# Optimization experiments

Measured on AMD Instinct MI355X. Metric: run time of the kernel, lower is better.

Reference implementation:

```python
import jax, jax.numpy as jnp
import numpy as np

D, H, DH, L, DFF, V, K = 512, 8, 64, 6, 2048, 256, 5
N = 10240
TAU = 0.1
EPS = 1e-5


def _ln(x, w, b):
    m = x.mean(-1, keepdims=True)
    v = ((x - m) ** 2).mean(-1, keepdims=True)
    return (x - m) * jax.lax.rsqrt(v + EPS) * w + b


def _attn(q_in, kv_in, inw, inb, ow, ob):
    # q_in: [Q, D], kv_in: [M, D]; standard PyTorch MultiheadAttention math
    wq, wk, wv = jnp.split(inw, 3, 0)
    bq, bk, bv = jnp.split(inb, 3)
    q = (q_in @ wq.T + bq).reshape(-1, H, DH)
    k = (kv_in @ wk.T + bk).reshape(-1, H, DH)
    v = (kv_in @ wv.T + bv).reshape(-1, H, DH)
    s = jnp.einsum('qhd,mhd->hqm', q, k) / np.float32(np.sqrt(DH))
    o = jnp.einsum('hqm,mhd->qhd', jax.nn.softmax(s, -1), v).reshape(-1, D)
    return o @ ow.T + ob


def setup_inputs() -> dict:
    key = jax.random.key(0)
    ks = iter(jax.random.split(key, 64))

    def w(shape):
        return jax.random.normal(next(ks), shape, jnp.float32) * 0.02

    inp = {
        'input_bytes': jax.random.randint(next(ks), (N,), 0, V, jnp.int32),
        'emb': w((V, D)),
        'alpha': jnp.float32(0.5),
        'enc_inw': w((L, 3 * D, D)), 'enc_inb': w((L, 3 * D)),
        'enc_ow': w((L, D, D)), 'enc_ob': w((L, D)),
        'enc_w1': w((L, DFF, D)), 'enc_b1': w((L, DFF)),
        'enc_w2': w((L, D, DFF)), 'enc_b2': w((L, D)),
        'enc_ln1w': jnp.ones((L, D)), 'enc_ln1b': jnp.zeros((L, D)),
        'enc_ln2w': jnp.ones((L, D)), 'enc_ln2b': jnp.zeros((L, D)),
        'dec_sa_inw': w((L, 3 * D, D)), 'dec_sa_inb': w((L, 3 * D)),
        'dec_sa_ow': w((L, D, D)), 'dec_sa_ob': w((L, D)),
        'dec_ca_inw': w((L, 3 * D, D)), 'dec_ca_inb': w((L, 3 * D)),
        'dec_ca_ow': w((L, D, D)), 'dec_ca_ob': w((L, D)),
        'dec_w1': w((L, DFF, D)), 'dec_b1': w((L, DFF)),
        'dec_w2': w((L, D, DFF)), 'dec_b2': w((L, D)),
        'dec_ln1w': jnp.ones((L, D)), 'dec_ln1b': jnp.zeros((L, D)),
        'dec_ln2w': jnp.ones((L, D)), 'dec_ln2b': jnp.zeros((L, D)),
        'dec_ln3w': jnp.ones((L, D)), 'dec_ln3b': jnp.zeros((L, D)),
        'out_w': w((V, D)), 'out_b': w((V,)),
    }
    return inp


def reference(input_bytes, emb, alpha, enc_inw, enc_inb, enc_ow, enc_ob,
              enc_w1, enc_b1, enc_w2, enc_b2, enc_ln1w, enc_ln1b, enc_ln2w, enc_ln2b,
              dec_sa_inw, dec_sa_inb, dec_sa_ow, dec_sa_ob,
              dec_ca_inw, dec_ca_inb, dec_ca_ow, dec_ca_ob,
              dec_w1, dec_b1, dec_w2, dec_b2,
              dec_ln1w, dec_ln1b, dec_ln2w, dec_ln2b, dec_ln3w, dec_ln3b,
              out_w, out_b):
    P = input_bytes.shape[0] // K
    patches = input_bytes[:P * K].reshape(P, K)            # fixed k-byte patching
    x = emb[patches].mean(1)                               # mean-pooled patch embeddings [P, D]
    # ---- TransformerEncoder (post-LN, relu FFN, no dropout at eval) ----
    for l in range(L):
        x = _ln(x + _attn(x, x, enc_inw[l], enc_inb[l], enc_ow[l], enc_ob[l]), enc_ln1w[l], enc_ln1b[l])
        ff = jax.nn.relu(x @ enc_w1[l].T + enc_b1[l]) @ enc_w2[l].T + enc_b2[l]
        x = _ln(x + ff, enc_ln2w[l], enc_ln2b[l])
    encoded = x                                            # [P, D]
    # ---- gating + embedding mix (vectorized over the per-patch loop) ----
    gate = jnp.linalg.norm(encoded, axis=-1) > TAU
    tok = emb[patches[:, -1]]
    x = jnp.where(gate[:, None], alpha * encoded + (1.0 - alpha) * tok, tok)  # [P, D]
    # ---- TransformerDecoder: each patch is an independent length-1 target;
    #      self-attn over a single token reduces to out_proj(V(x));
    #      cross-attn attends to the full encoded memory (as in the original loop) ----
    for l in range(L):
        wv = dec_sa_inw[l][2 * D:]
        bv = dec_sa_inb[l][2 * D:]
        sa = (x @ wv.T + bv) @ dec_sa_ow[l].T + dec_sa_ob[l]
        x = _ln(x + sa, dec_ln1w[l], dec_ln1b[l])
        ca = _attn(x, encoded, dec_ca_inw[l], dec_ca_inb[l], dec_ca_ow[l], dec_ca_ob[l])
        x = _ln(x + ca, dec_ln2w[l], dec_ln2b[l])
        ff = jax.nn.relu(x @ dec_w1[l].T + dec_b1[l]) @ dec_w2[l].T + dec_b2[l]
        x = _ln(x + ff, dec_ln3w[l], dec_ln3b[l])
    return x @ out_w.T + out_b                             # [P, V]
```

## Files before the change

### kernel.cpp

```cpp
#include <hip/hip_runtime.h>
#include <hip/hip_bf16.h>
#include <math.h>

#define DD   512
#define HN   8
#define DHD  64
#define LL   6
#define DFF_ 2048
#define VV   256
#define KB_  5
#define PP   2048
#define EPS_ 1e-5f
#define TAU_ 0.1f
#define NS   4
#define KVS  (PP / NS)

typedef __attribute__((ext_vector_type(8))) short bf16x8;
typedef __attribute__((ext_vector_type(4))) short bf16x4;
typedef __attribute__((ext_vector_type(4))) float f32x4;

__device__ __forceinline__ float wave_sum(float v) {
#pragma unroll
  for (int m = 32; m >= 1; m >>= 1) v += __shfl_xor(v, m, 64);
  return v;
}

__device__ __forceinline__ unsigned short f2bf(float f) {
  unsigned u = __float_as_uint(f);
  u += 0x7FFF + ((u >> 16) & 1);
  return (unsigned short)(u >> 16);
}

__device__ __forceinline__ bf16x8 cvt8(float4 a, float4 b) {
  bf16x8 v;
  v[0] = (short)f2bf(a.x); v[1] = (short)f2bf(a.y);
  v[2] = (short)f2bf(a.z); v[3] = (short)f2bf(a.w);
  v[4] = (short)f2bf(b.x); v[5] = (short)f2bf(b.y);
  v[6] = (short)f2bf(b.z); v[7] = (short)f2bf(b.w);
  return v;
}

__device__ __forceinline__ void gload16(const void* g, void* l) {
  __builtin_amdgcn_global_load_lds(
      (const __attribute__((address_space(1))) unsigned int*)g,
      (__attribute__((address_space(3))) unsigned int*)l, 16, 0, 0);
}

#define NSEG 55
struct CvtSeg { const float* src; short* dst; int n; };
struct CvtArgs { CvtSeg seg[NSEG]; };

__global__ __launch_bounds__(256) void convert_bf16_kernel(CvtArgs a) {
  const CvtSeg sg = a.seg[blockIdx.y];
  const int i = ((int)blockIdx.x * 256 + (int)threadIdx.x) * 8;
  if (i >= sg.n) return;
  const float4 x0 = *(const float4*)(sg.src + i);
  const float4 x1 = *(const float4*)(sg.src + i + 4);
  *(bf16x8*)(sg.dst + i) = cvt8(x0, x1);
}

__global__ __launch_bounds__(256) void transpose_wv_kernel(const float* __restrict__ sa_inw,
                                                           short* __restrict__ wvt) {
  __shared__ float t[64][65];
  const int l = blockIdx.z;
  const float* S = sa_inw + (size_t)l * 3 * DD * DD + (size_t)2 * DD * DD;
  short* D = wvt + (size_t)l * DD * DD;
  const int bo = blockIdx.y * 64;
  const int bi = blockIdx.x * 64;
  const int r = (int)threadIdx.x >> 2;
  const int c0 = ((int)threadIdx.x & 3) * 16;
#pragma unroll
  for (int j = 0; j < 16; j += 4)
    *(float4*)&t[r][c0 + j] = *(const float4*)&S[(size_t)(bo + r) * DD + bi + c0 + j];
  __syncthreads();
  bf16x8 o0, o1;
#pragma unroll
  for (int j = 0; j < 8; ++j) o0[j] = (short)f2bf(t[c0 + j][r]);
#pragma unroll
  for (int j = 0; j < 8; ++j) o1[j] = (short)f2bf(t[c0 + 8 + j][r]);
  short* dp = &D[(size_t)(bi + r) * DD + bo + c0];
  *(bf16x8*)dp = o0;
  *(bf16x8*)(dp + 8) = o1;
}

__global__ __launch_bounds__(256) void sa_bias_kernel(const float* __restrict__ sa_inb,
                                                      const float* __restrict__ sa_ow,
                                                      const float* __restrict__ sa_ob,
                                                      float* __restrict__ bc) {
  const int gid = (int)blockIdx.x * 4 + ((int)threadIdx.x >> 6);
  const int l = gid >> 9, n = gid & 511;
  const int lane = (int)threadIdx.x & 63;
  const float* wo = sa_ow + (size_t)l * DD * DD + (size_t)n * DD + lane * 8;
  const float* bv = sa_inb + (size_t)l * 3 * DD + 2 * DD + lane * 8;
  float s = 0.f;
#pragma unroll
  for (int j = 0; j < 8; ++j) s += wo[j] * bv[j];
  s = wave_sum(s);
  if (lane == 0) bc[(size_t)l * DD + n] = s + sa_ob[(size_t)l * DD + n];
}

__global__ __launch_bounds__(256) void gemm_wc_kernel(const short* __restrict__ WoBase,
                                                      size_t astr,
                                                      const short* __restrict__ WvT,
                                                      short* __restrict__ Wc) {
  constexpr int BK = 64;
  __shared__ short As[64 * BK];
  __shared__ short Bs[64 * BK];
  const int l = blockIdx.z;
  const short* A = WoBase + (size_t)l * astr;
  const short* W = WvT + (size_t)l * DD * DD;
  short* C = Wc + (size_t)l * DD * DD;
  const int tid = (int)threadIdx.x;
  const int lane = tid & 63;
  const int wid = tid >> 6;
  const int wm = (wid >> 1) * 32;
  const int wn = (wid & 1) * 32;
  const int bm = blockIdx.y * 64;
  const int bn = blockIdx.x * 64;
  const int fr = lane & 15;
  const int kq = lane >> 4;
  const int rs = fr & 7;
  const int srow = lane >> 3;
  const int scg = (lane & 7) ^ srow;

  f32x4 acc[2][2];
#pragma unroll
  for (int i = 0; i < 2; ++i)
#pragma unroll
    for (int j = 0; j < 2; ++j) acc[i][j] = (f32x4){0.f, 0.f, 0.f, 0.f};

  for (int k0 = 0; k0 < DD; k0 += BK) {
    __syncthreads();
#pragma unroll
    for (int is = 0; is < 2; ++is) {
      const int ib = is * 4 + wid;
      gload16(&A[(size_t)(bm + ib * 8 + srow) * DD + k0 + scg * 8], &As[ib * 512]);
      gload16(&W[(size_t)(bn + ib * 8 + srow) * DD + k0 + scg * 8], &Bs[ib * 512]);
    }
    __syncthreads();
#pragma unroll
    for (int s = 0; s < 2; ++s) {
      const int cg = s * 4 + kq;
      const int co = (cg ^ rs) * 8;
      bf16x8 af[2], bf[2];
#pragma unroll
      for (int i = 0; i < 2; ++i) af[i] = *(const bf16x8*)&As[(wm + i * 16 + fr) * BK + co];
#pragma unroll
      for (int j = 0; j < 2; ++j) bf[j] = *(const bf16x8*)&Bs[(wn + j * 16 + fr) * BK + co];
#pragma unroll
      for (int i = 0; i < 2; ++i)
#pragma unroll
        for (int j = 0; j < 2; ++j)
          acc[i][j] = __builtin_amdgcn_mfma_f32_16x16x32_bf16(af[i], bf[j], acc[i][j], 0, 0, 0);
    }
  }
  const int cr = (lane >> 4) * 4;
#pragma unroll
  for (int j = 0; j < 2; ++j) {
    const int col = bn + wn + j * 16 + fr;
#pragma unroll
    for (int i = 0; i < 2; ++i)
#pragma unroll
      for (int r = 0; r < 4; ++r)
        C[(size_t)(bm + wm + i * 16 + cr + r) * DD + col] = (short)f2bf(acc[i][j][r]);
  }
}

__global__ __launch_bounds__(256) void embed_mean_kernel(const int* __restrict__ bytes,
                                                         const float* __restrict__ emb,
                                                         float* __restrict__ x,
                                                         short* __restrict__ xb,
                                                         float* __restrict__ tok) {
  const int p = blockIdx.x;
  const int d = threadIdx.x * 2;
  float a0 = 0.f, a1 = 0.f;
  int last = 0;
#pragma unroll
  for (int k = 0; k < KB_; ++k) {
    const int idx = bytes[p * KB_ + k];
    last = idx;
    const float* e = emb + (size_t)idx * DD + d;
    a0 += e[0]; a1 += e[1];
  }
  a0 *= 0.2f; a1 *= 0.2f;
  x[(size_t)p * DD + d]     = a0;
  x[(size_t)p * DD + d + 1] = a1;
  xb[(size_t)p * DD + d]     = (short)f2bf(a0);
  xb[(size_t)p * DD + d + 1] = (short)f2bf(a1);
  const float* e = emb + (size_t)last * DD + d;
  tok[(size_t)p * DD + d]     = e[0];
  tok[(size_t)p * DD + d + 1] = e[1];
}

template <int BM, int BN, int NSPLIT, int RELU, int WF32, int WBF16, int QS>
__global__ __launch_bounds__(256) void gemm_gl_kernel(
    const short* __restrict__ A, int lda,
    const short* __restrict__ W, int ldw,
    const float* __restrict__ bias,
    float* __restrict__ Cf, short* __restrict__ Cb, int ldc, int Kd,
    size_t pstride) {
  constexpr int BK = 64;
  __shared__ short As[BM * BK];
  __shared__ short Bs[BN * BK];
  constexpr int WM = BM / 2, WN = BN / 2;
  constexpr int MF = WM / 16, NF = WN / 16;
  const int tid = (int)threadIdx.x;
  const int lane = tid & 63;
  const int wid = tid >> 6;
  const int wm = (wid >> 1) * WM;
  const int wn = (wid & 1) * WN;
  const int bm = blockIdx.y * BM;
  const int bn = blockIdx.x * BN;
  const int fr = lane & 15;
  const int kq = lane >> 4;
  const int rs = fr & 7;
  const int srow = lane >> 3;
  const int scg = (lane & 7) ^ srow;

  const int kz = (NSPLIT > 1) ? (int)blockIdx.z : 0;
  const int kbeg = kz * (Kd / NSPLIT);
  const int kend = kbeg + Kd / NSPLIT;

  f32x4 acc[MF][NF];
#pragma unroll
  for (int i = 0; i < MF; ++i)
#pragma unroll
    for (int j = 0; j < NF; ++j) acc[i][j] = (f32x4){0.f, 0.f, 0.f, 0.f};

  for (int k0 = kbeg; k0 < kend; k0 += BK) {
    __syncthreads();
#pragma unroll
    for (int is = 0; is < BM / 32; ++is) {
      const int ib = is * 4 + wid;
      gload16(&A[(size_t)(bm + ib * 8 + srow) * lda + k0 + scg * 8], &As[ib * 512]);
    }
#pragma unroll
    for (int is = 0; is < BN / 32; ++is) {
      const int ib = is * 4 + wid;
      gload16(&W[(size_t)(bn + ib * 8 + srow) * ldw + k0 + scg * 8], &Bs[ib * 512]);
    }
    __syncthreads();
#pragma unroll
    for (int s = 0; s < 2; ++s) {
      const int cg = s * 4 + kq;
      const int co = (cg ^ rs) * 8;
      bf16x8 af[MF], bf[NF];
#pragma unroll
      for (int i = 0; i < MF; ++i)
        af[i] = *(const bf16x8*)&As[(wm + i * 16 + fr) * BK + co];
#pragma unroll
      for (int j = 0; j < NF; ++j)
        bf[j] = *(const bf16x8*)&Bs[(wn + j * 16 + fr) * BK + co];
#pragma unroll
      for (int i = 0; i < MF; ++i)
#pragma unroll
        for (int j = 0; j < NF; ++j)
          acc[i][j] = __builtin_amdgcn_mfma_f32_16x16x32_bf16(af[i], bf[j], acc[i][j], 0, 0, 0);
    }
  }

  const int cr = (lane >> 4) * 4;
  if constexpr (NSPLIT > 1) {
    float* dst = Cf + (size_t)kz * pstride;
#pragma unroll
    for (int j = 0; j < NF; ++j) {
      const int col = bn + wn + j * 16 + fr;
#pragma unroll
      for (int i = 0; i < MF; ++i)
#pragma unroll
        for (int r = 0; r < 4; ++r)
          dst[(size_t)(bm + wm + i * 16 + cr + r) * ldc + col] = acc[i][j][r];
    }
  } else {
#pragma unroll
    for (int j = 0; j < NF; ++j) {
      const int col = bn + wn + j * 16 + fr;
      const float bb = bias[col];
      const float sc = (QS && col < DD) ? 0.125f : 1.f;
#pragma unroll
      for (int i = 0; i < MF; ++i) {
#pragma unroll
        for (int r = 0; r < 4; ++r) {
          float v = (acc[i][j][r] + bb) * sc;
          if (RELU) v = fmaxf(v, 0.f);
          const size_t idx = (size_t)(bm + wm + i * 16 + cr + r) * ldc + col;
          if (WF32) Cf[idx] = v;
          if (WBF16) Cb[idx] = (short)f2bf(v);
        }
      }
    }
  }
}

__global__ __launch_bounds__(256) void gemm_ca_kernel(
    const short* __restrict__ Aq, const short* __restrict__ Akv,
    const short* __restrict__ Wfull, const float* __restrict__ bias,
    short* __restrict__ Cb) {
  constexpr int BK = 64;
  __shared__ short As[64 * BK];
  __shared__ short Bs[64 * BK];
  const int bx = (int)blockIdx.x;
  const int part_kv = bx >= 8;
  const short* A = part_kv ? Akv : Aq;
  const int wrow0 = part_kv ? DD + (bx - 8) * 64 : bx * 64;
  const float sc = part_kv ? 1.f : 0.125f;
  const int tid = (int)threadIdx.x;
  const int lane = tid & 63;
  const int wid = tid >> 6;
  const int wm = (wid >> 1) * 32;
  const int wn = (wid & 1) * 32;
  const int bm = blockIdx.y * 64;
  const int fr = lane & 15;
  const int kq = lane >> 4;
  const int rs = fr & 7;
  const int srow = lane >> 3;
  const int scg = (lane & 7) ^ srow;

  f32x4 acc[2][2];
#pragma unroll
  for (int i = 0; i < 2; ++i)
#pragma unroll
    for (int j = 0; j < 2; ++j) acc[i][j] = (f32x4){0.f, 0.f, 0.f, 0.f};

  for (int k0 = 0; k0 < DD; k0 += BK) {
    __syncthreads();
#pragma unroll
    for (int is = 0; is < 2; ++is) {
      const int ib = is * 4 + wid;
      gload16(&A[(size_t)(bm + ib * 8 + srow) * DD + k0 + scg * 8], &As[ib * 512]);
      gload16(&Wfull[(size_t)(wrow0 + ib * 8 + srow) * DD + k0 + scg * 8], &Bs[ib * 512]);
    }
    __syncthreads();
#pragma unroll
    for (int s = 0; s < 2; ++s) {
      const int cg = s * 4 + kq;
      const int co = (cg ^ rs) * 8;
      bf16x8 af[2], bf[2];
#pragma unroll
      for (int i = 0; i < 2; ++i) af[i] = *(const bf16x8*)&As[(wm + i * 16 + fr) * BK + co];
#pragma unroll
      for (int j = 0; j < 2; ++j) bf[j] = *(const bf16x8*)&Bs[(wn + j * 16 + fr) * BK + co];
#pragma unroll
      for (int i = 0; i < 2; ++i)
#pragma unroll
        for (int j = 0; j < 2; ++j)
          acc[i][j] = __builtin_amdgcn_mfma_f32_16x16x32_bf16(af[i], bf[j], acc[i][j], 0, 0, 0);
    }
  }
  const int cr = (lane >> 4) * 4;
#pragma unroll
  for (int j = 0; j < 2; ++j) {
    const int col = wrow0 + wn + j * 16 + fr;
    const float bb = bias[col];
#pragma unroll
    for (int i = 0; i < 2; ++i)
#pragma unroll
      for (int r = 0; r < 4; ++r)
        Cb[(size_t)(bm + wm + i * 16 + cr + r) * (3 * DD) + col] =
            (short)f2bf((acc[i][j][r] + bb) * sc);
  }
}

__global__ __launch_bounds__(256) void flash_attn_mfma_kernel(const short* __restrict__ qkvb,
                                                              float* __restrict__ Opart,
                                                              float* __restrict__ stats) {
  constexpr int LS = 72;
  __shared__ short Ks[64 * LS];
  __shared__ short Vt[64 * LS];
  __shared__ short Ps[64 * LS];
  const int h = blockIdx.y;
  const int q0 = blockIdx.x * 64;
  const int sp = blockIdx.z;
  const int tid = (int)threadIdx.x;
  const int lane = tid & 63;
  const int wid = tid >> 6;
  const int fr = lane & 15;
  const int g = lane >> 4;
  const int kg = g * 8;

  bf16x8 qf[2];
  {
    const short* src = qkvb + (size_t)(q0 + wid * 16 + fr) * (3 * DD) + h * DHD + kg;
    qf[0] = *(const bf16x8*)src;
    qf[1] = *(const bf16x8*)(src + 32);
  }

  f32x4 acc_o[4];
#pragma unroll
  for (int df = 0; df < 4; ++df) acc_o[df] = (f32x4){0.f, 0.f, 0.f, 0.f};
  float mreg = -INFINITY, lsum = 0.f;

  const int sr8 = tid >> 3;
  const int sc8 = (tid & 7) * 8;
  const int vk2 = (tid & 31) * 2;
  const int vd8 = (tid >> 5) * 8;

  for (int t = 0; t < KVS / 64; ++t) {
    const int k0 = sp * KVS + t * 64;
    __syncthreads();
    {
#pragma unroll
      for (int p = 0; p < 64; p += 32)
        *(bf16x8*)&Ks[(sr8 + p) * LS + sc8] =
            *(const bf16x8*)&qkvb[(size_t)(k0 + sr8 + p) * (3 * DD) + DD + h * DHD + sc8];
      const short* vbase = qkvb + (size_t)(k0 + vk2) * (3 * DD) + 2 * DD + h * DHD + vd8;
      const bf16x8 v0 = *(const bf16x8*)vbase;
      const bf16x8 v1 = *(const bf16x8*)(vbase + 3 * DD);
#pragma unroll
      for (int j = 0; j < 8; ++j) {
        const unsigned pk = ((unsigned)(unsigned short)v0[j]) |
                            (((unsigned)(unsigned short)v1[j]) << 16);
        *(unsigned*)&Vt[(vd8 + j) * LS + vk2] = pk;
      }
    }
    __syncthreads();

    f32x4 st[4];
#pragma unroll
    for (int nf = 0; nf < 4; ++nf) st[nf] = (f32x4){0.f, 0.f, 0.f, 0.f};
    __builtin_amdgcn_s_setprio(1);
#pragma unroll
    for (int nf = 0; nf < 4; ++nf) {
      const bf16x8 kf0 = *(const bf16x8*)&Ks[(nf * 16 + fr) * LS + kg];
      const bf16x8 kf1 = *(const bf16x8*)&Ks[(nf * 16 + fr) * LS + kg + 32];
      st[nf] = __builtin_amdgcn_mfma_f32_16x16x32_bf16(kf0, qf[0], st[nf], 0, 0, 0);
      st[nf] = __builtin_amdgcn_mfma_f32_16x16x32_bf16(kf1, qf[1], st[nf], 0, 0, 0);
    }
    __builtin_amdgcn_s_setprio(0);

    float mx = st[0][0];
#pragma unroll
    for (int nf = 0; nf < 4; ++nf)
#pragma unroll
      for (int i = 0; i < 4; ++i) mx = fmaxf(mx, st[nf][i]);
    mx = fmaxf(mx, __shfl_xor(mx, 16, 64));
    mx = fmaxf(mx, __shfl_xor(mx, 32, 64));
    const float mn = fmaxf(mreg, mx);
    const float corr = __expf(mreg - mn);
    mreg = mn;
    float pv[4][4];
    float sum = 0.f;
#pragma unroll
    for (int nf = 0; nf < 4; ++nf)
#pragma unroll
      for (int i = 0; i < 4; ++i) {
        pv[nf][i] = __expf(st[nf][i] - mn);
        sum += pv[nf][i];
      }
    sum += __shfl_xor(sum, 16, 64);
    sum += __shfl_xor(sum, 32, 64);
    lsum = lsum * corr + sum;

    float corr_acc[4];
#pragma unroll
    for (int i = 0; i < 4; ++i)
      corr_acc[i] = __shfl(corr, (lane & 48) | (g * 4 + i), 64);
#pragma unroll
    for (int df = 0; df < 4; ++df) {
      acc_o[df][0] *= corr_acc[0]; acc_o[df][1] *= corr_acc[1];
      acc_o[df][2] *= corr_acc[2]; acc_o[df][3] *= corr_acc[3];
    }

#pragma unroll
    for (int nf = 0; nf < 4; ++nf) {
      bf16x4 pw;
#pragma unroll
      for (int i = 0; i < 4; ++i) pw[i] = (short)f2bf(pv[nf][i]);
      *(bf16x4*)&Ps[(wid * 16 + fr) * LS + nf * 16 + g * 4] = pw;
    }
    asm volatile("s_waitcnt lgkmcnt(0)" ::: "memory");

    const bf16x8 pa0 = *(const bf16x8*)&Ps[(wid * 16 + fr) * LS + kg];
    const bf16x8 pa1 = *(const bf16x8*)&Ps[(wid * 16 + fr) * LS + kg + 32];
    __builtin_amdgcn_s_setprio(1);
#pragma unroll
    for (int df = 0; df < 4; ++df) {
      const bf16x8 vb0 = *(const bf16x8*)&Vt[(df * 16 + fr) * LS + kg];
      const bf16x8 vb1 = *(const bf16x8*)&Vt[(df * 16 + fr) * LS + kg + 32];
      acc_o[df] = __builtin_amdgcn_mfma_f32_16x16x32_bf16(pa0, vb0, acc_o[df], 0, 0, 0);
      acc_o[df] = __builtin_amdgcn_mfma_f32_16x16x32_bf16(pa1, vb1, acc_o[df], 0, 0, 0);
    }
    __builtin_amdgcn_s_setprio(0);
  }

  const int orow = q0 + wid * 16 + g * 4;
#pragma unroll
  for (int df = 0; df < 4; ++df)
#pragma unroll
    for (int i = 0; i < 4; ++i)
      Opart[((size_t)sp * PP + orow + i) * DD + h * DHD + df * 16 + fr] = acc_o[df][i];
  if (g == 0) {
    const size_t si = (((size_t)sp * PP + q0 + wid * 16 + fr) * HN + h) * 2;
    stats[si]     = mreg;
    stats[si + 1] = lsum;
  }
}

__global__ __launch_bounds__(256) void attn_combine_kernel(const float* __restrict__ Opart,
                                                           const float* __restrict__ stats,
                                                           short* __restrict__ outb) {
  const int row = blockIdx.x;
  const int d = (int)threadIdx.x * 2;
  const int h = d >> 6;
  float m[NS], l[NS];
  float M = -INFINITY;
#pragma unroll
  for (int s = 0; s < NS; ++s) {
    const size_t si = (((size_t)s * PP + row) * HN + h) * 2;
    m[s] = stats[si]; l[s] = stats[si + 1];
    M = fmaxf(M, m[s]);
  }
  float L = 0.f, o0 = 0.f, o1 = 0.f;
#pragma unroll
  for (int s = 0; s < NS; ++s) {
    const float e = __expf(m[s] - M);
    L += l[s] * e;
    const float* op = Opart + ((size_t)s * PP + row) * DD + d;
    o0 += op[0] * e;
    o1 += op[1] * e;
  }
  const float inv = 1.f / L;
  outb[(size_t)row * DD + d]     = (short)f2bf(o0 * inv);
  outb[(size_t)row * DD + d + 1] = (short)f2bf(o1 * inv);
}

__global__ __launch_bounds__(256) void ln_residual_kernel(const float* __restrict__ xin,
                                                          const float* __restrict__ pA,
                                                          const float* __restrict__ pB,
                                                          const float* __restrict__ gb,
                                                          const float* __restrict__ w,
                                                          const float* __restrict__ b,
                                                          float* __restrict__ out,
                                                          short* __restrict__ outb) {
  const int row = blockIdx.x * 4 + (threadIdx.x >> 6);
  const int lane = threadIdx.x & 63;
  const size_t base = (size_t)row * DD + lane * 8;
  float v[8];
  {
    const float4 a0 = *(const float4*)&xin[base];
    const float4 a1 = *(const float4*)&xin[base + 4];
    const float4 r0 = *(const float4*)&pA[base];
    const float4 r1 = *(const float4*)&pA[base + 4];
    const float4 s0 = *(const float4*)&pB[base];
    const float4 s1 = *(const float4*)&pB[base + 4];
    const float4 g0 = *(const float4*)&gb[lane * 8];
    const float4 g1 = *(const float4*)&gb[lane * 8 + 4];
    v[0] = a0.x + r0.x + s0.x + g0.x; v[1] = a0.y + r0.y + s0.y + g0.y;
    v[2] = a0.z + r0.z + s0.z + g0.z; v[3] = a0.w + r0.w + s0.w + g0.w;
    v[4] = a1.x + r1.x + s1.x + g1.x; v[5] = a1.y + r1.y + s1.y + g1.y;
    v[6] = a1.z + r1.z + s1.z + g1.z; v[7] = a1.w + r1.w + s1.w + g1.w;
  }
  float sum = 0.f;
#pragma unroll
  for (int j = 0; j < 8; ++j) sum += v[j];
  sum = wave_sum(sum);
  const float mean = sum * (1.f / DD);
  float sq = 0.f;
#pragma unroll
  for (int j = 0; j < 8; ++j) { const float dd = v[j] - mean; sq += dd * dd; }
  sq = wave_sum(sq);
  const float rstd = rsqrtf(sq * (1.f / DD) + EPS_);
  const float* wp = w + lane * 8;
  const float* bp = b + lane * 8;
  float o[8];
#pragma unroll
  for (int j = 0; j < 8; ++j) o[j] = (v[j] - mean) * rstd * wp[j] + bp[j];
  *(float4*)&out[base] = *(float4*)&o[0];
  *(float4*)&out[base + 4] = *(float4*)&o[4];
  bf16x8 ob;
#pragma unroll
  for (int j = 0; j < 8; ++j) ob[j] = (short)f2bf(o[j]);
  *(bf16x8*)&outb[base] = ob;
}

__global__ __launch_bounds__(256) void gate_mix_kernel(const float* __restrict__ tok,
                                                       const float* __restrict__ alpha_p,
                                                       float* __restrict__ x,
                                                       short* __restrict__ xb,
                                                       short* __restrict__ encb) {
  const int row = blockIdx.x * 4 + (threadIdx.x >> 6);
  const int lane = threadIdx.x & 63;
  const size_t base = (size_t)row * DD + lane * 8;
  float e[8], t[8];
  {
    const float4 a0 = *(const float4*)&x[base];
    const float4 a1 = *(const float4*)&x[base + 4];
    const float4 b0 = *(const float4*)&tok[base];
    const float4 b1 = *(const float4*)&tok[base + 4];
    e[0] = a0.x; e[1] = a0.y; e[2] = a0.z; e[3] = a0.w;
    e[4] = a1.x; e[5] = a1.y; e[6] = a1.z; e[7] = a1.w;
    t[0] = b0.x; t[1] = b0.y; t[2] = b0.z; t[3] = b0.w;
    t[4] = b1.x; t[5] = b1.y; t[6] = b1.z; t[7] = b1.w;
  }
  bf16x8 eb;
#pragma unroll
  for (int j = 0; j < 8; ++j) eb[j] = (short)f2bf(e[j]);
  *(bf16x8*)&encb[base] = eb;
  float sq = 0.f;
#pragma unroll
  for (int j = 0; j < 8; ++j) sq += e[j] * e[j];
  sq = wave_sum(sq);
  const bool gate = sq > TAU_ * TAU_;
  const float a = *alpha_p;
  float o[8];
#pragma unroll
  for (int j = 0; j < 8; ++j) o[j] = gate ? (a * e[j] + (1.f - a) * t[j]) : t[j];
  *(float4*)&x[base] = *(float4*)&o[0];
  *(float4*)&x[base + 4] = *(float4*)&o[4];
  bf16x8 ob;
#pragma unroll
  for (int j = 0; j < 8; ++j) ob[j] = (short)f2bf(o[j]);
  *(bf16x8*)&xb[base] = ob;
}

__global__ __launch_bounds__(256) void out_combine_kernel(const float* __restrict__ P0,
                                                          const float* __restrict__ P1,
                                                          const float* __restrict__ bias,
                                                          float* __restrict__ out) {
  const size_t i = ((size_t)blockIdx.x * 256 + threadIdx.x) * 4;
  const int col = (int)(i % VV);
  const float4 a = *(const float4*)&P0[i];
  const float4 b = *(const float4*)&P1[i];
  const float4 c = *(const float4*)&bias[col];
  float4 o;
  o.x = a.x + b.x + c.x; o.y = a.y + b.y + c.y;
  o.z = a.z + b.z + c.z; o.w = a.w + b.w + c.w;
  *(float4*)&out[i] = o;
}

extern "C" void kernel_launch(void* const* d_in, const int* in_sizes, int n_in,
                              void* d_out, int out_size, void* d_ws, size_t ws_size,
                              hipStream_t stream) {
  const int*   bytes    = (const int*)d_in[0];
  const float* emb      = (const float*)d_in[1];
  const float* alpha    = (const float*)d_in[2];
  const float* enc_inw  = (const float*)d_in[3];
  const float* enc_inb  = (const float*)d_in[4];
  const float* enc_ow   = (const float*)d_in[5];
  const float* enc_ob   = (const float*)d_in[6];
  const float* enc_w1   = (const float*)d_in[7];
  const float* enc_b1   = (const float*)d_in[8];
  const float* enc_w2   = (const float*)d_in[9];
  const float* enc_b2   = (const float*)d_in[10];
  const float* enc_ln1w = (const float*)d_in[11];
  const float* enc_ln1b = (const float*)d_in[12];
  const float* enc_ln2w = (const float*)d_in[13];
  const float* enc_ln2b = (const float*)d_in[14];
  const float* dec_sa_inw = (const float*)d_in[15];
  const float* dec_sa_inb = (const float*)d_in[16];
  const float* dec_sa_ow  = (const float*)d_in[17];
  const float* dec_sa_ob  = (const float*)d_in[18];
  const float* dec_ca_inw = (const float*)d_in[19];
  const float* dec_ca_inb = (const float*)d_in[20];
  const float* dec_ca_ow  = (const float*)d_in[21];
  const float* dec_ca_ob  = (const float*)d_in[22];
  const float* dec_w1   = (const float*)d_in[23];
  const float* dec_b1   = (const float*)d_in[24];
  const float* dec_w2   = (const float*)d_in[25];
  const float* dec_b2   = (const float*)d_in[26];
  const float* dec_ln1w = (const float*)d_in[27];
  const float* dec_ln1b = (const float*)d_in[28];
  const float* dec_ln2w = (const float*)d_in[29];
  const float* dec_ln2b = (const float*)d_in[30];
  const float* dec_ln3w = (const float*)d_in[31];
  const float* dec_ln3b = (const float*)d_in[32];
  const float* out_w    = (const float*)d_in[33];
  const float* out_b    = (const float*)d_in[34];

  float* fp = (float*)d_ws;
  float* x     = fp;  fp += (size_t)PP * DD;
  float* tok   = fp;  fp += (size_t)PP * DD;
  float* Opart = fp;  fp += (size_t)NS * PP * DD;
  float* stats = fp;  fp += (size_t)NS * PP * HN * 2;
  float* tmpP  = fp;  fp += (size_t)2 * PP * DD;
  float* outP  = fp;  fp += (size_t)2 * PP * VV;
  float* bcbuf = fp;  fp += (size_t)LL * DD;
  short* sp = (short*)fp;
  short* x_bf    = sp;  sp += (size_t)PP * DD;
  short* enc_bf  = sp;  sp += (size_t)PP * DD;
  short* qkv_bf  = sp;  sp += (size_t)PP * 3 * DD;
  short* attno_bf= sp;  sp += (size_t)PP * DFF_;
  short* ffh_bf  = sp;  sp += (size_t)PP * DFF_;
  short* wvT     = sp;  sp += (size_t)LL * DD * DD;
  short* wcM     = sp;  sp += (size_t)LL * DD * DD;
  short* warena  = sp;

  CvtArgs ca;
  size_t eoff[LL][4], doff[LL][5], ooff;
  size_t dec_start = 0, dec_stride = 0;
  {
    int si = 0;
    size_t off = 0;
    const size_t n0 = 3 * DD * DD, n1 = DD * DD, n2 = (size_t)DFF_ * DD, n3 = (size_t)DD * DFF_;
    for (int l = 0; l < LL; ++l) {
      ca.seg[si++] = {enc_inw + (size_t)l * n0, warena + off, (int)n0}; eoff[l][0] = off; off += n0;
      ca.seg[si++] = {enc_ow  + (size_t)l * n1, warena + off, (int)n1}; eoff[l][1] = off; off += n1;
      ca.seg[si++] = {enc_w1  + (size_t)l * n2, warena + off, (int)n2}; eoff[l][2] = off; off += n2;
      ca.seg[si++] = {enc_w2  + (size_t)l * n3, warena + off, (int)n3}; eoff[l][3] = off; off += n3;
    }
    dec_start = off;
    for (int l = 0; l < LL; ++l) {
      const size_t o0 = off;
      ca.seg[si++] = {dec_sa_ow  + (size_t)l * n1, warena + off, (int)n1}; doff[l][0] = off; off += n1;
      ca.seg[si++] = {dec_ca_inw + (size_t)l * n0, warena + off, (int)n0}; doff[l][1] = off; off += n0;
      ca.seg[si++] = {dec_ca_ow  + (size_t)l * n1, warena + off, (int)n1}; doff[l][2] = off; off += n1;
      ca.seg[si++] = {dec_w1     + (size_t)l * n2, warena + off, (int)n2}; doff[l][3] = off; off += n2;
      ca.seg[si++] = {dec_w2     + (size_t)l * n3, warena + off, (int)n3}; doff[l][4] = off; off += n3;
      if (l == 0) dec_stride = off - o0; (void)o0;
    }
    ca.seg[si++] = {out_w, warena + off, VV * DD}; ooff = off;
  }

  const dim3 b256(256);
  const dim3 gFA(PP / 64, HN, NS);
  const dim3 gQKV(3 * DD / 64, PP / 128);
  const dim3 gFF1(DFF_ / 64, PP / 128);
  const dim3 gS(DD / 64, PP / 64, 2);
  const dim3 gCA(24, PP / 64);
  const dim3 gOUTg(VV / 64, PP / 64, 2);
  const size_t psD = (size_t)PP * DD;
  const size_t psV = (size_t)PP * VV;

  convert_bf16_kernel<<<dim3(512, NSEG), b256, 0, stream>>>(ca);
  transpose_wv_kernel<<<dim3(8, 8, LL), b256, 0, stream>>>(dec_sa_inw, wvT);
  sa_bias_kernel<<<(LL * DD) / 4, b256, 0, stream>>>(dec_sa_inb, dec_sa_ow, dec_sa_ob, bcbuf);
  gemm_wc_kernel<<<dim3(8, 8, LL), b256, 0, stream>>>(warena + dec_start, dec_stride, wvT, wcM);
  embed_mean_kernel<<<PP, b256, 0, stream>>>(bytes, emb, x, x_bf, tok);

  for (int l = 0; l < LL; ++l) {
    const float* inb = enc_inb + (size_t)l * 3 * DD;
    const float* ob  = enc_ob  + (size_t)l * DD;
    const float* b1  = enc_b1  + (size_t)l * DFF_;
    const float* b2  = enc_b2  + (size_t)l * DD;

    gemm_gl_kernel<128, 64, 1, 0, 0, 1, 1><<<gQKV, b256, 0, stream>>>(
        x_bf, DD, warena + eoff[l][0], DD, inb, nullptr, qkv_bf, 3 * DD, DD, 0);
    flash_attn_mfma_kernel<<<gFA, b256, 0, stream>>>(qkv_bf, Opart, stats);
    attn_combine_kernel<<<PP, b256, 0, stream>>>(Opart, stats, attno_bf);
    gemm_gl_kernel<64, 64, 2, 0, 1, 0, 0><<<gS, b256, 0, stream>>>(
        attno_bf, DD, warena + eoff[l][1], DD, nullptr, tmpP, nullptr, DD, DD, psD);
    ln_residual_kernel<<<PP / 4, b256, 0, stream>>>(
        x, tmpP, tmpP + psD, ob, enc_ln1w + (size_t)l * DD, enc_ln1b + (size_t)l * DD, x, x_bf);
    gemm_gl_kernel<128, 64, 1, 1, 0, 1, 0><<<gFF1, b256, 0, stream>>>(
        x_bf, DD, warena + eoff[l][2], DD, b1, nullptr, ffh_bf, DFF_, DD, 0);
    gemm_gl_kernel<64, 64, 2, 0, 1, 0, 0><<<gS, b256, 0, stream>>>(
        ffh_bf, DFF_, warena + eoff[l][3], DFF_, nullptr, tmpP, nullptr, DD, DFF_, psD);
    ln_residual_kernel<<<PP / 4, b256, 0, stream>>>(
        x, tmpP, tmpP + psD, b2, enc_ln2w + (size_t)l * DD, enc_ln2b + (size_t)l * DD, x, x_bf);
  }

  gate_mix_kernel<<<PP / 4, b256, 0, stream>>>(tok, alpha, x, x_bf, enc_bf);

  for (int l = 0; l < LL; ++l) {
    const float* ca_inb = dec_ca_inb + (size_t)l * 3 * DD;
    const float* ca_ob  = dec_ca_ob + (size_t)l * DD;
    const float* b1 = dec_b1 + (size_t)l * DFF_;
    const float* b2 = dec_b2 + (size_t)l * DD;

    gemm_gl_kernel<64, 64, 2, 0, 1, 0, 0><<<gS, b256, 0, stream>>>(
        x_bf, DD, wcM + (size_t)l * DD * DD, DD, nullptr, tmpP, nullptr, DD, DD, psD);
    ln_residual_kernel<<<PP / 4, b256, 0, stream>>>(
        x, tmpP, tmpP + psD, bcbuf + (size_t)l * DD,
        dec_ln1w + (size_t)l * DD, dec_ln1b + (size_t)l * DD, x, x_bf);

    gemm_ca_kernel<<<gCA, b256, 0, stream>>>(
        x_bf, enc_bf, warena + doff[l][1], ca_inb, qkv_bf);
    flash_attn_mfma_kernel<<<gFA, b256, 0, stream>>>(qkv_bf, Opart, stats);
    attn_combine_kernel<<<PP, b256, 0, stream>>>(Opart, stats, attno_bf);
    gemm_gl_kernel<64, 64, 2, 0, 1, 0, 0><<<gS, b256, 0, stream>>>(
        attno_bf, DD, warena + doff[l][2], DD, nullptr, tmpP, nullptr, DD, DD, psD);
    ln_residual_kernel<<<PP / 4, b256, 0, stream>>>(
        x, tmpP, tmpP + psD, ca_ob, dec_ln2w + (size_t)l * DD, dec_ln2b + (size_t)l * DD, x, x_bf);

    gemm_gl_kernel<128, 64, 1, 1, 0, 1, 0><<<gFF1, b256, 0, stream>>>(
        x_bf, DD, warena + doff[l][3], DD, b1, nullptr, ffh_bf, DFF_, DD, 0);
    gemm_gl_kernel<64, 64, 2, 0, 1, 0, 0><<<gS, b256, 0, stream>>>(
        ffh_bf, DFF_, warena + doff[l][4], DFF_, nullptr, tmpP, nullptr, DD, DFF_, psD);
    ln_residual_kernel<<<PP / 4, b256, 0, stream>>>(
        x, tmpP, tmpP + psD, b2, dec_ln3w + (size_t)l * DD, dec_ln3b + (size_t)l * DD, x, x_bf);
  }

  gemm_gl_kernel<64, 64, 2, 0, 1, 0, 0><<<gOUTg, b256, 0, stream>>>(
      x_bf, DD, warena + ooff, DD, nullptr, outP, nullptr, VV, DD, psV);
  out_combine_kernel<<<(PP * VV / 4) / 256, b256, 0, stream>>>(
      outP, outP + psV, out_b, (float*)d_out);
}
```

Measured before the change: 1.110 ms.

## Fuse split-KV attention combine into out-projection GEMM A-tile load

```diff
diff --git a/kernel.cpp b/kernel.cpp
--- a/kernel.cpp
+++ b/kernel.cpp
@@ -52,11 +52,14 @@
 
 __global__ __launch_bounds__(256) void convert_bf16_kernel(CvtArgs a) {
   const CvtSeg sg = a.seg[blockIdx.y];
-  const int i = ((int)blockIdx.x * 256 + (int)threadIdx.x) * 8;
+  const int i = ((int)blockIdx.x * 256 + (int)threadIdx.x) * 16;
   if (i >= sg.n) return;
   const float4 x0 = *(const float4*)(sg.src + i);
   const float4 x1 = *(const float4*)(sg.src + i + 4);
-  *(bf16x8*)(sg.dst + i) = cvt8(x0, x1);
+  const float4 x2 = *(const float4*)(sg.src + i + 8);
+  const float4 x3 = *(const float4*)(sg.src + i + 12);
+  *(bf16x8*)(sg.dst + i)     = cvt8(x0, x1);
+  *(bf16x8*)(sg.dst + i + 8) = cvt8(x2, x3);
 }
 
 __global__ __launch_bounds__(256) void transpose_wv_kernel(const float* __restrict__ sa_inw,
@@ -292,6 +295,114 @@
   }
 }
 
+__global__ __launch_bounds__(256) void gemm_ao_kernel(
+    const float* __restrict__ Opart, const float* __restrict__ stats,
+    const short* __restrict__ W, float* __restrict__ Cf, size_t pstride) {
+  constexpr int BK = 64;
+  __shared__ short As[64 * BK];
+  __shared__ short Bs[64 * BK];
+  const int tid = (int)threadIdx.x;
+  const int lane = tid & 63;
+  const int wid = tid >> 6;
+  const int wm = (wid >> 1) * 32;
+  const int wn = (wid & 1) * 32;
+  const int bm = blockIdx.y * 64;
+  const int bn = blockIdx.x * 64;
+  const int fr = lane & 15;
+  const int kq = lane >> 4;
+  const int rs = fr & 7;
+  const int srow = lane >> 3;
+  const int scg = (lane & 7) ^ srow;
+  const int arow = tid >> 2;
+  const int acg0 = (tid & 3) * 2;
+  const int ad0 = acg0 * 8;
+
+  const int kz = (int)blockIdx.z;
+  const int kbeg = kz * (DD / 2);
+
+  f32x4 acc[2][2];
+#pragma unroll
+  for (int i = 0; i < 2; ++i)
+#pragma unroll
+    for (int j = 0; j < 2; ++j) acc[i][j] = (f32x4){0.f, 0.f, 0.f, 0.f};
+
+  for (int t = 0; t < 4; ++t) {
+    const int k0 = kbeg + t * BK;
+    const int h = k0 >> 6;
+    __syncthreads();
+#pragma unroll
+    for (int is = 0; is < 2; ++is) {
+      const int ib = is * 4 + wid;
+      gload16(&W[(size_t)(bn + ib * 8 + srow) * DD + k0 + scg * 8], &Bs[ib * 512]);
+    }
+    {
+      const int row = bm + arow;
+      float mm[NS], ll[NS];
+      float M = -INFINITY;
+#pragma unroll
+      for (int s = 0; s < NS; ++s) {
+        const size_t si = (((size_t)s * PP + row) * HN + h) * 2;
+        mm[s] = stats[si]; ll[s] = stats[si + 1];
+        M = fmaxf(M, mm[s]);
+      }
+      float L = 0.f, e[NS];
+#pragma unroll
+      for (int s = 0; s < NS; ++s) { e[s] = __expf(mm[s] - M); L += ll[s] * e[s]; }
+      const float inv = 1.f / L;
+      float o[16];
+#pragma unroll
+      for (int j = 0; j < 16; ++j) o[j] = 0.f;
+#pragma unroll
+      for (int s = 0; s < NS; ++s) {
+        const float sc = e[s] * inv;
+        const float* op = Opart + ((size_t)s * PP + row) * DD + k0 + ad0;
+        const float4 a0 = *(const float4*)op;
+        const float4 a1 = *(const float4*)(op + 4);
+        const float4 a2 = *(const float4*)(op + 8);
+        const float4 a3 = *(const float4*)(op + 12);
+        o[0]  += a0.x * sc; o[1]  += a0.y * sc; o[2]  += a0.z * sc; o[3]  += a0.w * sc;
+        o[4]  += a1.x * sc; o[5]  += a1.y * sc; o[6]  += a1.z * sc; o[7]  += a1.w * sc;
+        o[8]  += a2.x * sc; o[9]  += a2.y * sc; o[10] += a2.z * sc; o[11] += a2.w * sc;
+        o[12] += a3.x * sc; o[13] += a3.y * sc; o[14] += a3.z * sc; o[15] += a3.w * sc;
+      }
+      bf16x8 lo, hi;
+#pragma unroll
+      for (int j = 0; j < 8; ++j) { lo[j] = (short)f2bf(o[j]); hi[j] = (short)f2bf(o[8 + j]); }
+      const int r7 = arow & 7;
+      *(bf16x8*)&As[arow * BK + ((acg0 ^ r7) << 3)]       = lo;
+      *(bf16x8*)&As[arow * BK + (((acg0 + 1) ^ r7) << 3)] = hi;
+    }
+    __syncthreads();
+#pragma unroll
+    for (int s = 0; s < 2; ++s) {
+      const int cg = s * 4 + kq;
+      const int co = (cg ^ rs) * 8;
+      bf16x8 af[2], bf[2];
+#pragma unroll
+      for (int i = 0; i < 2; ++i) af[i] = *(const bf16x8*)&As[(wm + i * 16 + fr) * BK + co];
+#pragma unroll
+      for (int j = 0; j < 2; ++j) bf[j] = *(const bf16x8*)&Bs[(wn + j * 16 + fr) * BK + co];
+#pragma unroll
+      for (int i = 0; i < 2; ++i)
+#pragma unroll
+        for (int j = 0; j < 2; ++j)
+          acc[i][j] = __builtin_amdgcn_mfma_f32_16x16x32_bf16(af[i], bf[j], acc[i][j], 0, 0, 0);
+    }
+  }
+
+  const int cr = (lane >> 4) * 4;
+  float* dst = Cf + (size_t)kz * pstride;
+#pragma unroll
+  for (int j = 0; j < 2; ++j) {
+    const int col = bn + wn + j * 16 + fr;
+#pragma unroll
+    for (int i = 0; i < 2; ++i)
+#pragma unroll
+      for (int r = 0; r < 4; ++r)
+        dst[(size_t)(bm + wm + i * 16 + cr + r) * DD + col] = acc[i][j][r];
+  }
+}
+
 __global__ __launch_bounds__(256) void gemm_ca_kernel(
     const short* __restrict__ Aq, const short* __restrict__ Akv,
     const short* __restrict__ Wfull, const float* __restrict__ bias,
@@ -451,14 +562,10 @@
     sum += __shfl_xor(sum, 32, 64);
     lsum = lsum * corr + sum;
 
-    float corr_acc[4];
-#pragma unroll
-    for (int i = 0; i < 4; ++i)
-      corr_acc[i] = __shfl(corr, (lane & 48) | (g * 4 + i), 64);
 #pragma unroll
     for (int df = 0; df < 4; ++df) {
-      acc_o[df][0] *= corr_acc[0]; acc_o[df][1] *= corr_acc[1];
-      acc_o[df][2] *= corr_acc[2]; acc_o[df][3] *= corr_acc[3];
+      acc_o[df][0] *= corr; acc_o[df][1] *= corr;
+      acc_o[df][2] *= corr; acc_o[df][3] *= corr;
     }
 
 #pragma unroll
@@ -470,58 +577,29 @@
     }
     asm volatile("s_waitcnt lgkmcnt(0)" ::: "memory");
 
-    const bf16x8 pa0 = *(const bf16x8*)&Ps[(wid * 16 + fr) * LS + kg];
-    const bf16x8 pa1 = *(const bf16x8*)&Ps[(wid * 16 + fr) * LS + kg + 32];
+    const bf16x8 pb0 = *(const bf16x8*)&Ps[(wid * 16 + fr) * LS + kg];
+    const bf16x8 pb1 = *(const bf16x8*)&Ps[(wid * 16 + fr) * LS + kg + 32];
     __builtin_amdgcn_s_setprio(1);
 #pragma unroll
     for (int df = 0; df < 4; ++df) {
-      const bf16x8 vb0 = *(const bf16x8*)&Vt[(df * 16 + fr) * LS + kg];
-      const bf16x8 vb1 = *(const bf16x8*)&Vt[(df * 16 + fr) * LS + kg + 32];
-      acc_o[df] = __builtin_amdgcn_mfma_f32_16x16x32_bf16(pa0, vb0, acc_o[df], 0, 0, 0);
-      acc_o[df] = __builtin_amdgcn_mfma_f32_16x16x32_bf16(pa1, vb1, acc_o[df], 0, 0, 0);
+      const bf16x8 va0 = *(const bf16x8*)&Vt[(df * 16 + fr) * LS + kg];
+      const bf16x8 va1 = *(const bf16x8*)&Vt[(df * 16 + fr) * LS + kg + 32];
+      acc_o[df] = __builtin_amdgcn_mfma_f32_16x16x32_bf16(va0, pb0, acc_o[df], 0, 0, 0);
+      acc_o[df] = __builtin_amdgcn_mfma_f32_16x16x32_bf16(va1, pb1, acc_o[df], 0, 0, 0);
     }
     __builtin_amdgcn_s_setprio(0);
   }
 
-  const int orow = q0 + wid * 16 + g * 4;
+  const int q = q0 + wid * 16 + fr;
+  float* obase = Opart + ((size_t)sp * PP + q) * DD + h * DHD + g * 4;
 #pragma unroll
   for (int df = 0; df < 4; ++df)
-#pragma unroll
-    for (int i = 0; i < 4; ++i)
-      Opart[((size_t)sp * PP + orow + i) * DD + h * DHD + df * 16 + fr] = acc_o[df][i];
+    *(f32x4*)&obase[df * 16] = acc_o[df];
   if (g == 0) {
-    const size_t si = (((size_t)sp * PP + q0 + wid * 16 + fr) * HN + h) * 2;
+    const size_t si = (((size_t)sp * PP + q) * HN + h) * 2;
     stats[si]     = mreg;
     stats[si + 1] = lsum;
   }
-}
-
-__global__ __launch_bounds__(256) void attn_combine_kernel(const float* __restrict__ Opart,
-                                                           const float* __restrict__ stats,
-                                                           short* __restrict__ outb) {
-  const int row = blockIdx.x;
-  const int d = (int)threadIdx.x * 2;
-  const int h = d >> 6;
-  float m[NS], l[NS];
-  float M = -INFINITY;
-#pragma unroll
-  for (int s = 0; s < NS; ++s) {
-    const size_t si = (((size_t)s * PP + row) * HN + h) * 2;
-    m[s] = stats[si]; l[s] = stats[si + 1];
-    M = fmaxf(M, m[s]);
-  }
-  float L = 0.f, o0 = 0.f, o1 = 0.f;
-#pragma unroll
-  for (int s = 0; s < NS; ++s) {
-    const float e = __expf(m[s] - M);
-    L += l[s] * e;
-    const float* op = Opart + ((size_t)s * PP + row) * DD + d;
-    o0 += op[0] * e;
-    o1 += op[1] * e;
-  }
-  const float inv = 1.f / L;
-  outb[(size_t)row * DD + d]     = (short)f2bf(o0 * inv);
-  outb[(size_t)row * DD + d + 1] = (short)f2bf(o1 * inv);
 }
 
 __global__ __launch_bounds__(256) void ln_residual_kernel(const float* __restrict__ xin,
@@ -679,7 +757,6 @@
   short* x_bf    = sp;  sp += (size_t)PP * DD;
   short* enc_bf  = sp;  sp += (size_t)PP * DD;
   short* qkv_bf  = sp;  sp += (size_t)PP * 3 * DD;
-  short* attno_bf= sp;  sp += (size_t)PP * DFF_;
   short* ffh_bf  = sp;  sp += (size_t)PP * DFF_;
   short* wvT     = sp;  sp += (size_t)LL * DD * DD;
   short* wcM     = sp;  sp += (size_t)LL * DD * DD;
@@ -721,7 +798,7 @@
   const size_t psD = (size_t)PP * DD;
   const size_t psV = (size_t)PP * VV;
 
-  convert_bf16_kernel<<<dim3(512, NSEG), b256, 0, stream>>>(ca);
+  convert_bf16_kernel<<<dim3(256, NSEG), b256, 0, stream>>>(ca);
   transpose_wv_kernel<<<dim3(8, 8, LL), b256, 0, stream>>>(dec_sa_inw, wvT);
   sa_bias_kernel<<<(LL * DD) / 4, b256, 0, stream>>>(dec_sa_inb, dec_sa_ow, dec_sa_ob, bcbuf);
   gemm_wc_kernel<<<dim3(8, 8, LL), b256, 0, stream>>>(warena + dec_start, dec_stride, wvT, wcM);
@@ -736,9 +813,8 @@
     gemm_gl_kernel<128, 64, 1, 0, 0, 1, 1><<<gQKV, b256, 0, stream>>>(
         x_bf, DD, warena + eoff[l][0], DD, inb, nullptr, qkv_bf, 3 * DD, DD, 0);
     flash_attn_mfma_kernel<<<gFA, b256, 0, stream>>>(qkv_bf, Opart, stats);
-    attn_combine_kernel<<<PP, b256, 0, stream>>>(Opart, stats, attno_bf);
-    gemm_gl_kernel<64, 64, 2, 0, 1, 0, 0><<<gS, b256, 0, stream>>>(
-        attno_bf, DD, warena + eoff[l][1], DD, nullptr, tmpP, nullptr, DD, DD, psD);
+    gemm_ao_kernel<<<gS, b256, 0, stream>>>(
+        Opart, stats, warena + eoff[l][1], tmpP, psD);
     ln_residual_kernel<<<PP / 4, b256, 0, stream>>>(
         x, tmpP, tmpP + psD, ob, enc_ln1w + (size_t)l * DD, enc_ln1b + (size_t)l * DD, x, x_bf);
     gemm_gl_kernel<128, 64, 1, 1, 0, 1, 0><<<gFF1, b256, 0, stream>>>(
@@ -766,9 +842,8 @@
     gemm_ca_kernel<<<gCA, b256, 0, stream>>>(
         x_bf, enc_bf, warena + doff[l][1], ca_inb, qkv_bf);
     flash_attn_mfma_kernel<<<gFA, b256, 0, stream>>>(qkv_bf, Opart, stats);
-    attn_combine_kernel<<<PP, b256, 0, stream>>>(Opart, stats, attno_bf);
-    gemm_gl_kernel<64, 64, 2, 0, 1, 0, 0><<<gS, b256, 0, stream>>>(
-        attno_bf, DD, warena + doff[l][2], DD, nullptr, tmpP, nullptr, DD, DD, psD);
+    gemm_ao_kernel<<<gS, b256, 0, stream>>>(
+        Opart, stats, warena + doff[l][2], tmpP, psD);
     ln_residual_kernel<<<PP / 4, b256, 0, stream>>>(
         x, tmpP, tmpP + psD, ca_ob, dec_ln2w + (size_t)l * DD, dec_ln2b + (size_t)l * DD, x, x_bf);
 
```

Measured after the change: 1.300 ms. +17.2%, slower.

## Process 128 queries per flash-attention block to reuse K/V tiles

Applied to the files above, without the earlier changes.

```diff
diff --git a/kernel.cpp b/kernel.cpp
--- a/kernel.cpp
+++ b/kernel.cpp
@@ -52,11 +52,14 @@
 
 __global__ __launch_bounds__(256) void convert_bf16_kernel(CvtArgs a) {
   const CvtSeg sg = a.seg[blockIdx.y];
-  const int i = ((int)blockIdx.x * 256 + (int)threadIdx.x) * 8;
+  const int i = ((int)blockIdx.x * 256 + (int)threadIdx.x) * 16;
   if (i >= sg.n) return;
   const float4 x0 = *(const float4*)(sg.src + i);
   const float4 x1 = *(const float4*)(sg.src + i + 4);
-  *(bf16x8*)(sg.dst + i) = cvt8(x0, x1);
+  const float4 x2 = *(const float4*)(sg.src + i + 8);
+  const float4 x3 = *(const float4*)(sg.src + i + 12);
+  *(bf16x8*)(sg.dst + i)     = cvt8(x0, x1);
+  *(bf16x8*)(sg.dst + i + 8) = cvt8(x2, x3);
 }
 
 __global__ __launch_bounds__(256) void transpose_wv_kernel(const float* __restrict__ sa_inw,
@@ -367,9 +370,9 @@
   constexpr int LS = 72;
   __shared__ short Ks[64 * LS];
   __shared__ short Vt[64 * LS];
-  __shared__ short Ps[64 * LS];
+  __shared__ short Ps[128 * LS];
   const int h = blockIdx.y;
-  const int q0 = blockIdx.x * 64;
+  const int q0 = blockIdx.x * 128;
   const int sp = blockIdx.z;
   const int tid = (int)threadIdx.x;
   const int lane = tid & 63;
@@ -378,17 +381,21 @@
   const int g = lane >> 4;
   const int kg = g * 8;
 
-  bf16x8 qf[2];
-  {
-    const short* src = qkvb + (size_t)(q0 + wid * 16 + fr) * (3 * DD) + h * DHD + kg;
-    qf[0] = *(const bf16x8*)src;
-    qf[1] = *(const bf16x8*)(src + 32);
-  }
-
-  f32x4 acc_o[4];
-#pragma unroll
-  for (int df = 0; df < 4; ++df) acc_o[df] = (f32x4){0.f, 0.f, 0.f, 0.f};
-  float mreg = -INFINITY, lsum = 0.f;
+  bf16x8 qf[2][2];
+#pragma unroll
+  for (int qs = 0; qs < 2; ++qs) {
+    const short* src = qkvb + (size_t)(q0 + qs * 64 + wid * 16 + fr) * (3 * DD) + h * DHD + kg;
+    qf[qs][0] = *(const bf16x8*)src;
+    qf[qs][1] = *(const bf16x8*)(src + 32);
+  }
+
+  f32x4 acc_o[2][4];
+#pragma unroll
+  for (int qs = 0; qs < 2; ++qs)
+#pragma unroll
+    for (int df = 0; df < 4; ++df) acc_o[qs][df] = (f32x4){0.f, 0.f, 0.f, 0.f};
+  float mreg[2] = {-INFINITY, -INFINITY};
+  float lsum[2] = {0.f, 0.f};
 
   const int sr8 = tid >> 3;
   const int sc8 = (tid & 7) * 8;
@@ -415,84 +422,95 @@
     }
     __syncthreads();
 
-    f32x4 st[4];
-#pragma unroll
-    for (int nf = 0; nf < 4; ++nf) st[nf] = (f32x4){0.f, 0.f, 0.f, 0.f};
+    float corr_acc[2][4];
+#pragma unroll
+    for (int qs = 0; qs < 2; ++qs) {
+      f32x4 st[4];
+#pragma unroll
+      for (int nf = 0; nf < 4; ++nf) st[nf] = (f32x4){0.f, 0.f, 0.f, 0.f};
+      __builtin_amdgcn_s_setprio(1);
+#pragma unroll
+      for (int nf = 0; nf < 4; ++nf) {
+        const bf16x8 kf0 = *(const bf16x8*)&Ks[(nf * 16 + fr) * LS + kg];
+        const bf16x8 kf1 = *(const bf16x8*)&Ks[(nf * 16 + fr) * LS + kg + 32];
+        st[nf] = __builtin_amdgcn_mfma_f32_16x16x32_bf16(kf0, qf[qs][0], st[nf], 0, 0, 0);
+        st[nf] = __builtin_amdgcn_mfma_f32_16x16x32_bf16(kf1, qf[qs][1], st[nf], 0, 0, 0);
+      }
+      __builtin_amdgcn_s_setprio(0);
+
+      float mx = st[0][0];
+#pragma unroll
+      for (int nf = 0; nf < 4; ++nf)
+#pragma unroll
+        for (int i = 0; i < 4; ++i) mx = fmaxf(mx, st[nf][i]);
+      mx = fmaxf(mx, __shfl_xor(mx, 16, 64));
+      mx = fmaxf(mx, __shfl_xor(mx, 32, 64));
+      const float mn = fmaxf(mreg[qs], mx);
+      const float corr = __expf(mreg[qs] - mn);
+      mreg[qs] = mn;
+      float pvv[4][4];
+      float sum = 0.f;
+#pragma unroll
+      for (int nf = 0; nf < 4; ++nf)
+#pragma unroll
+        for (int i = 0; i < 4; ++i) {
+          pvv[nf][i] = __expf(st[nf][i] - mn);
+          sum += pvv[nf][i];
+        }
+      sum += __shfl_xor(sum, 16, 64);
+      sum += __shfl_xor(sum, 32, 64);
+      lsum[qs] = lsum[qs] * corr + sum;
+
+#pragma unroll
+      for (int i = 0; i < 4; ++i)
+        corr_acc[qs][i] = __shfl(corr, (lane & 48) | (g * 4 + i), 64);
+
+#pragma unroll
+      for (int nf = 0; nf < 4; ++nf) {
+        bf16x4 pw;
+#pragma unroll
+        for (int i = 0; i < 4; ++i) pw[i] = (short)f2bf(pvv[nf][i]);
+        *(bf16x4*)&Ps[(qs * 64 + wid * 16 + fr) * LS + nf * 16 + g * 4] = pw;
+      }
+    }
+    asm volatile("s_waitcnt lgkmcnt(0)" ::: "memory");
+
     __builtin_amdgcn_s_setprio(1);
 #pragma unroll
-    for (int nf = 0; nf < 4; ++nf) {
-      const bf16x8 kf0 = *(const bf16x8*)&Ks[(nf * 16 + fr) * LS + kg];
-      const bf16x8 kf1 = *(const bf16x8*)&Ks[(nf * 16 + fr) * LS + kg + 32];
-      st[nf] = __builtin_amdgcn_mfma_f32_16x16x32_bf16(kf0, qf[0], st[nf], 0, 0, 0);
-      st[nf] = __builtin_amdgcn_mfma_f32_16x16x32_bf16(kf1, qf[1], st[nf], 0, 0, 0);
+    for (int qs = 0; qs < 2; ++qs) {
+#pragma unroll
+      for (int df = 0; df < 4; ++df) {
+        acc_o[qs][df][0] *= corr_acc[qs][0];
+        acc_o[qs][df][1] *= corr_acc[qs][1];
+        acc_o[qs][df][2] *= corr_acc[qs][2];
+        acc_o[qs][df][3] *= corr_acc[qs][3];
+      }
+      const bf16x8 pa0 = *(const bf16x8*)&Ps[(qs * 64 + wid * 16 + fr) * LS + kg];
+      const bf16x8 pa1 = *(const bf16x8*)&Ps[(qs * 64 + wid * 16 + fr) * LS + kg + 32];
+#pragma unroll
+      for (int df = 0; df < 4; ++df) {
+        const bf16x8 vb0 = *(const bf16x8*)&Vt[(df * 16 + fr) * LS + kg];
+        const bf16x8 vb1 = *(const bf16x8*)&Vt[(df * 16 + fr) * LS + kg + 32];
+        acc_o[qs][df] = __builtin_amdgcn_mfma_f32_16x16x32_bf16(pa0, vb0, acc_o[qs][df], 0, 0, 0);
+        acc_o[qs][df] = __builtin_amdgcn_mfma_f32_16x16x32_bf16(pa1, vb1, acc_o[qs][df], 0, 0, 0);
+      }
     }
     __builtin_amdgcn_s_setprio(0);
-
-    float mx = st[0][0];
-#pragma unroll
-    for (int nf = 0; nf < 4; ++nf)
-#pragma unroll
-      for (int i = 0; i < 4; ++i) mx = fmaxf(mx, st[nf][i]);
-    mx = fmaxf(mx, __shfl_xor(mx, 16, 64));
-    mx = fmaxf(mx, __shfl_xor(mx, 32, 64));
-    const float mn = fmaxf(mreg, mx);
-    const float corr = __expf(mreg - mn);
-    mreg = mn;
-    float pv[4][4];
-    float sum = 0.f;
-#pragma unroll
-    for (int nf = 0; nf < 4; ++nf)
-#pragma unroll
-      for (int i = 0; i < 4; ++i) {
-        pv[nf][i] = __expf(st[nf][i] - mn);
-        sum += pv[nf][i];
-      }
-    sum += __shfl_xor(sum, 16, 64);
-    sum += __shfl_xor(sum, 32, 64);
-    lsum = lsum * corr + sum;
-
-    float corr_acc[4];
-#pragma unroll
-    for (int i = 0; i < 4; ++i)
-      corr_acc[i] = __shfl(corr, (lane & 48) | (g * 4 + i), 64);
-#pragma unroll
-    for (int df = 0; df < 4; ++df) {
-      acc_o[df][0] *= corr_acc[0]; acc_o[df][1] *= corr_acc[1];
-      acc_o[df][2] *= corr_acc[2]; acc_o[df][3] *= corr_acc[3];
-    }
-
-#pragma unroll
-    for (int nf = 0; nf < 4; ++nf) {
-      bf16x4 pw;
-#pragma unroll
-      for (int i = 0; i < 4; ++i) pw[i] = (short)f2bf(pv[nf][i]);
-      *(bf16x4*)&Ps[(wid * 16 + fr) * LS + nf * 16 + g * 4] = pw;
-    }
-    asm volatile("s_waitcnt lgkmcnt(0)" ::: "memory");
-
-    const bf16x8 pa0 = *(const bf16x8*)&Ps[(wid * 16 + fr) * LS + kg];
-    const bf16x8 pa1 = *(const bf16x8*)&Ps[(wid * 16 + fr) * LS + kg + 32];
-    __builtin_amdgcn_s_setprio(1);
-#pragma unroll
-    for (int df = 0; df < 4; ++df) {
-      const bf16x8 vb0 = *(const bf16x8*)&Vt[(df * 16 + fr) * LS + kg];
-      const bf16x8 vb1 = *(const bf16x8*)&Vt[(df * 16 + fr) * LS + kg + 32];
-      acc_o[df] = __builtin_amdgcn_mfma_f32_16x16x32_bf16(pa0, vb0, acc_o[df], 0, 0, 0);
-      acc_o[df] = __builtin_amdgcn_mfma_f32_16x16x32_bf16(pa1, vb1, acc_o[df], 0, 0, 0);
-    }
-    __builtin_amdgcn_s_setprio(0);
-  }
-
-  const int orow = q0 + wid * 16 + g * 4;
-#pragma unroll
-  for (int df = 0; df < 4; ++df)
-#pragma unroll
-    for (int i = 0; i < 4; ++i)
-      Opart[((size_t)sp * PP + orow + i) * DD + h * DHD + df * 16 + fr] = acc_o[df][i];
-  if (g == 0) {
-    const size_t si = (((size_t)sp * PP + q0 + wid * 16 + fr) * HN + h) * 2;
-    stats[si]     = mreg;
-    stats[si + 1] = lsum;
+  }
+
+#pragma unroll
+  for (int qs = 0; qs < 2; ++qs) {
+    const int orow = q0 + qs * 64 + wid * 16 + g * 4;
+#pragma unroll
+    for (int df = 0; df < 4; ++df)
+#pragma unroll
+      for (int i = 0; i < 4; ++i)
+        Opart[((size_t)sp * PP + orow + i) * DD + h * DHD + df * 16 + fr] = acc_o[qs][df][i];
+    if (g == 0) {
+      const size_t si = (((size_t)sp * PP + q0 + qs * 64 + wid * 16 + fr) * HN + h) * 2;
+      stats[si]     = mreg[qs];
+      stats[si + 1] = lsum[qs];
+    }
   }
 }
 
@@ -679,7 +697,7 @@
   short* x_bf    = sp;  sp += (size_t)PP * DD;
   short* enc_bf  = sp;  sp += (size_t)PP * DD;
   short* qkv_bf  = sp;  sp += (size_t)PP * 3 * DD;
-  short* attno_bf= sp;  sp += (size_t)PP * DFF_;
+  short* attno_bf= sp;  sp += (size_t)PP * DD;
   short* ffh_bf  = sp;  sp += (size_t)PP * DFF_;
   short* wvT     = sp;  sp += (size_t)LL * DD * DD;
   short* wcM     = sp;  sp += (size_t)LL * DD * DD;
@@ -712,7 +730,7 @@
   }
 
   const dim3 b256(256);
-  const dim3 gFA(PP / 64, HN, NS);
+  const dim3 gFA(PP / 128, HN, NS);
   const dim3 gQKV(3 * DD / 64, PP / 128);
   const dim3 gFF1(DFF_ / 64, PP / 128);
   const dim3 gS(DD / 64, PP / 64, 2);
@@ -721,7 +739,7 @@
   const size_t psD = (size_t)PP * DD;
   const size_t psV = (size_t)PP * VV;
 
-  convert_bf16_kernel<<<dim3(512, NSEG), b256, 0, stream>>>(ca);
+  convert_bf16_kernel<<<dim3(256, NSEG), b256, 0, stream>>>(ca);
   transpose_wv_kernel<<<dim3(8, 8, LL), b256, 0, stream>>>(dec_sa_inw, wvT);
   sa_bias_kernel<<<(LL * DD) / 4, b256, 0, stream>>>(dec_sa_inb, dec_sa_ow, dec_sa_ob, bcbuf);
   gemm_wc_kernel<<<dim3(8, 8, LL), b256, 0, stream>>>(warena + dec_start, dec_stride, wvT, wcM);
```

Result: slower. 1.147 ms (+3.4%).
